# Performance work log

Measured on AMD Instinct MI355X. Metric: run time of the kernel, lower is better.

The kernel has to match this reference:

```python
import jax, jax.numpy as jnp
import numpy as np

SOM = (32, 32)   # som_dim; SOM[0]*SOM[1] == num_embeddings
LR = 0.05


def setup_inputs() -> dict:
    key = jax.random.key(0)
    k1, k2 = jax.random.split(key)
    B, K, D = 65536, 1024, 256
    x = jax.random.normal(k1, (B, D), dtype=jnp.float32)
    embeddings = jax.random.uniform(k2, (K, D), dtype=jnp.float32)  # torch.rand init
    return {"x": x, "embeddings": embeddings}


def reference(x, embeddings):
    K, D = embeddings.shape
    # pairwise squared distances: [B, K]
    dist = (jnp.sum(x * x, axis=1, keepdims=True)
            + jnp.sum(embeddings * embeddings, axis=1)
            - 2.0 * (x @ embeddings.T))
    n_min = jnp.argmin(dist, axis=1)          # [B]
    z_q = embeddings[n_min]                   # [B, D]

    # SOM grid coordinates and clamped neighbors
    n_x = n_min // SOM[1]
    n_y = n_min % SOM[1]
    x_up = jnp.where(n_x < SOM[0] - 1, n_x + 1, n_x)
    x_down = jnp.where(n_x > 0, n_x - 1, n_x)
    y_right = jnp.where(n_y < SOM[1] - 1, n_y + 1, n_y)
    y_left = jnp.where(n_y > 0, n_y - 1, n_y)
    idx_up = x_up * SOM[1] + n_y
    idx_down = x_down * SOM[1] + n_y
    idx_right = n_x * SOM[1] + y_right
    idx_left = n_x * SOM[1] + y_left

    # [B, 4, D] neighbor gather (order: up, down, left, right as in torch code)
    nbr_idx = jnp.stack([idx_up, idx_down, idx_left, idx_right], axis=1)
    z_q_neighbors = embeddings[nbr_idx]

    # SOM scatter update (torch does one-hot matmuls; segment_sum is the fused form)
    dw = x - z_q                              # [B, D]
    seg = lambda idx: jax.ops.segment_sum(dw, idx, num_segments=K)
    new_embeddings = jax.lax.stop_gradient(
        embeddings
        + LR * seg(n_min)
        + 0.5 * LR * (seg(idx_up) + seg(idx_down) + seg(idx_right) + seg(idx_left))
    )

    commit_loss = jnp.mean((x - z_q) ** 2)
    som_loss = jnp.mean((jax.lax.stop_gradient(x)[:, None, :] - z_q_neighbors) ** 2)
    return z_q, commit_loss, som_loss, new_embeddings
```

## Files before the change

kernel.cpp:

```cpp
#include <hip/hip_runtime.h>

#define B_ROWS 65536
#define DDIM   256
#define KEMB   1024
#define LRC    0.05f
#define BM 128

typedef __attribute__((ext_vector_type(8))) _Float16 half8;
typedef __attribute__((ext_vector_type(4))) float f32x4;

#define SX_OFF    0u
#define CNT_OFF   1048576u
#define SUMS_OFF  1052672u
#define ESQ_OFF   1053312u
#define CUR_OFF   1057408u
#define NMIN_OFF  1061504u
#define ROWS_OFF  1585792u
#define EH_OFF    1847936u

static __device__ __forceinline__ unsigned short f2h(float f) {
  _Float16 h = (_Float16)f;
  return *(unsigned short*)&h;
}
static __device__ __forceinline__ float h2f(unsigned short u) {
  _Float16 h = *(_Float16*)&u;
  return (float)h;
}
static __device__ __forceinline__ void glds16(const void* g, void* l) {
  __builtin_amdgcn_global_load_lds(
      (const __attribute__((address_space(1))) unsigned int*)g,
      (__attribute__((address_space(3))) unsigned int*)l, 16, 0, 0);
}

__global__ __launch_bounds__(256) void convert_kernel(
    const float* __restrict__ X, const float* __restrict__ E,
    unsigned short* __restrict__ outU, unsigned short* __restrict__ Eh,
    float* __restrict__ esq, double* __restrict__ sums) {
  __shared__ float red[256];
  const size_t nX8 = (size_t)B_ROWS * DDIM / 8;
  size_t i = (size_t)blockIdx.x * 256 + threadIdx.x;
  bool isX = (i < nX8);
  const float* src;
  unsigned short *dh, *dl = nullptr;
  if (isX) {
    size_t off = i * 8;
    src = X + off;
    dh = outU + (off >> 8) * 512 + (off & 255);
    dl = dh + 256;
  } else {
    size_t off = (i - nX8) * 8;
    src = E + off;
    dh = Eh + off;
  }
  const float4 v0 = *(const float4*)src;
  const float4 v1 = *(const float4*)(src + 4);
  float f[8] = {v0.x, v0.y, v0.z, v0.w, v1.x, v1.y, v1.z, v1.w};
  unsigned short h[8], l[8];
  float part = 0.f;
#pragma unroll
  for (int j = 0; j < 8; ++j) {
    h[j] = f2h(f[j]);
    l[j] = f2h(f[j] - h2f(h[j]));
    part += f[j] * f[j];
  }
  *(uint4*)dh = *(const uint4*)h;
  if (isX) *(uint4*)dl = *(const uint4*)l;
  if (!isX) {
    float s = part;
    for (int off = 16; off > 0; off >>= 1) s += __shfl_down(s, off, 32);
    if ((threadIdx.x & 31) == 0) esq[(i - nX8) >> 5] = s;
  }
  red[threadIdx.x] = isX ? part : 0.f;
  __syncthreads();
  for (int s = 128; s > 0; s >>= 1) {
    if (threadIdx.x < s) red[threadIdx.x] += red[threadIdx.x + s];
    __syncthreads();
  }
  if (threadIdx.x == 0 && isX)
    atomicAdd(&sums[8 + ((int)blockIdx.x & 63)], (double)red[0]);
}

__global__ __launch_bounds__(256, 1) void gemm_argmin_kernel(
    const unsigned short* __restrict__ XhlU, const unsigned short* __restrict__ EhW,
    const float* __restrict__ esq, const float* __restrict__ Ef,
    int* __restrict__ nmin, int* __restrict__ counts, float* __restrict__ zq) {
  __shared__ __align__(16) unsigned short sX[2][8][512][8];
  __shared__ __align__(16) unsigned short sE[2][512][8];

  const int tid  = threadIdx.x;
  const int lane = tid & 63, w = tid >> 6;
  const int lrow = lane & 15;
  const int qidx = lane >> 4;
  const int rowbase = (w >> 1) * 64;
  const int colb    = (w & 1) * 64;
  const int bm0 = (int)blockIdx.x * BM;

  int ec_row[2], ec_q8[2];
#pragma unroll
  for (int j = 0; j < 2; ++j) {
    const int c = j * 256 + tid;
    ec_row[j] = c >> 2;
    ec_q8[j]  = ((c & 3) ^ ((ec_row[j] >> 1) & 3)) * 8;
  }

#pragma unroll
  for (int j = 0; j < 2; ++j) {
    const int c = j * 256 + tid;
    glds16(EhW + (size_t)ec_row[j] * DDIM + ec_q8[j], (char*)&sE[0][c][0]);
  }
#pragma unroll
  for (int it = 0; it < 32; ++it) {
    const int c    = it * 256 + tid;
    const int tile = c >> 12;
    const int kcc  = (c >> 9) & 7;
    const int cc   = c & 511;
    const int row  = cc >> 2;
    const int q    = (cc & 3) ^ ((row >> 1) & 3);
    glds16(XhlU + (size_t)(bm0 + row) * 512 + tile * 256 + kcc * 32 + q * 8,
           (char*)sX + (size_t)c * 16);
  }

  float rbest[16];
  int   ridx[16];
#pragma unroll
  for (int i = 0; i < 16; ++i) { rbest[i] = 3.4e38f; ridx[i] = 0; }

  __syncthreads();

  for (int nt = 0; nt < 8; ++nt) {
    f32x4 acc[4][4];
#pragma unroll
    for (int i = 0; i < 4; ++i)
#pragma unroll
      for (int j = 0; j < 4; ++j) acc[i][j] = (f32x4){0.f, 0.f, 0.f, 0.f};

#pragma unroll
    for (int kcc = 0; kcc < 8; ++kcc) {
      const int s   = nt * 8 + kcc;
      const int cur = s & 1;
      if (s < 63) {
        const int ns = s + 1;
        const int nnt = ns >> 3, nk = ns & 7;
#pragma unroll
        for (int j = 0; j < 2; ++j) {
          const int c = j * 256 + tid;
          glds16(EhW + (size_t)(nnt * BM + ec_row[j]) * DDIM + nk * 32 + ec_q8[j],
                 (char*)&sE[cur ^ 1][c][0]);
        }
      }
      half8 af0[4], af1[4], bfr[4];
#pragma unroll
      for (int t = 0; t < 4; ++t) {
        const int m  = rowbase + t * 16 + lrow;
        const int sa = qidx ^ ((m >> 1) & 3);
        af0[t] = *(const half8*)&sX[0][kcc][(m << 2) | sa][0];
        af1[t] = *(const half8*)&sX[1][kcc][(m << 2) | sa][0];
        const int n  = colb + t * 16 + lrow;
        const int sb = qidx ^ ((n >> 1) & 3);
        bfr[t] = *(const half8*)&sE[cur][(n << 2) | sb][0];
      }
#pragma unroll
      for (int tr = 0; tr < 4; ++tr)
#pragma unroll
        for (int tc = 0; tc < 4; ++tc)
          acc[tr][tc] = __builtin_amdgcn_mfma_f32_16x16x32_f16(
              af0[tr], bfr[tc], acc[tr][tc], 0, 0, 0);
#pragma unroll
      for (int tr = 0; tr < 4; ++tr)
#pragma unroll
        for (int tc = 0; tc < 4; ++tc)
          acc[tr][tc] = __builtin_amdgcn_mfma_f32_16x16x32_f16(
              af1[tr], bfr[tc], acc[tr][tc], 0, 0, 0);
      __syncthreads();
    }
#pragma unroll
    for (int tc = 0; tc < 4; ++tc) {
      const int col = nt * BM + colb + tc * 16 + lrow;
      const float eq = esq[col];
#pragma unroll
      for (int tr = 0; tr < 4; ++tr)
#pragma unroll
        for (int rr = 0; rr < 4; ++rr) {
          float d = eq - 2.0f * acc[tr][tc][rr];
          const int slot = tr * 4 + rr;
          if (d < rbest[slot]) { rbest[slot] = d; ridx[slot] = col; }
        }
    }
  }

  float* cdd = (float*)&sE[0][0][0];
  int*   cdi = (int*)(cdd + 256);
  int*   snm = cdi + 256;
  int*   h   = (int*)&sX[0][0][0][0];

#pragma unroll
  for (int i = 0; i < 4; ++i) h[tid + i * 256] = 0;

#pragma unroll
  for (int slot = 0; slot < 16; ++slot) {
    float bd = rbest[slot];
    int   bi = ridx[slot];
#pragma unroll
    for (int off = 1; off < 16; off <<= 1) {
      float od = __shfl_xor(bd, off, 64);
      int   oi = __shfl_xor(bi, off, 64);
      if (od < bd || (od == bd && oi < bi)) { bd = od; bi = oi; }
    }
    if (lrow == 0) {
      const int row = rowbase + (slot >> 2) * 16 + (lane >> 4) * 4 + (slot & 3);
      cdd[(w & 1) * 128 + row] = bd;
      cdi[(w & 1) * 128 + row] = bi;
    }
  }
  __syncthreads();
  if (tid < BM) {
    float d0 = cdd[tid], d1 = cdd[128 + tid];
    int   i0 = cdi[tid], i1 = cdi[128 + tid];
    int bi = (d1 < d0 || (d1 == d0 && i1 < i0)) ? i1 : i0;
    nmin[bm0 + tid] = bi;
    snm[tid] = bi;
    atomicAdd(&h[bi], 1);
  }
  __syncthreads();
#pragma unroll
  for (int i = 0; i < 4; ++i) {
    int v = h[tid + i * 256];
    if (v) atomicAdd(&counts[tid + i * 256], v);
  }
  const int r0 = w * 32;
#pragma unroll 4
  for (int r = 0; r < 32; ++r) {
    const int k = snm[r0 + r];
    const float4 v = *(const float4*)(Ef + (size_t)k * DDIM + lane * 4);
    *(float4*)(zq + (size_t)(bm0 + r0 + r) * DDIM + lane * 4) = v;
  }
}

__global__ __launch_bounds__(1024) void scan_kernel(
    const int* __restrict__ counts, int* __restrict__ cur) {
  __shared__ int tmp[KEMB];
  int tid = threadIdx.x;
  int v = counts[tid];
  tmp[tid] = v;
  __syncthreads();
  for (int off = 1; off < 1024; off <<= 1) {
    int u = (tid >= off) ? tmp[tid - off] : 0;
    __syncthreads();
    tmp[tid] += u;
    __syncthreads();
  }
  cur[tid] = tmp[tid] - v;
}

__global__ __launch_bounds__(1024) void scatter_kernel(
    const int* __restrict__ nm, int* __restrict__ cur,
    int* __restrict__ rows) {
  __shared__ int lcnt[KEMB], lbase[KEMB], lrank[KEMB];
  int tid = threadIdx.x;
  lcnt[tid] = 0; lrank[tid] = 0;
  __syncthreads();
  int b = blockIdx.x * 1024 + tid;
  int k = nm[b];
  atomicAdd(&lcnt[k], 1);
  __syncthreads();
  if (lcnt[tid] > 0) lbase[tid] = atomicAdd(&cur[tid], lcnt[tid]);
  __syncthreads();
  int r = atomicAdd(&lrank[k], 1);
  rows[lbase[k] + r] = b;
}

__global__ __launch_bounds__(256) void sxsum_kernel(
    const int* __restrict__ rows, const int* __restrict__ nm,
    const float* __restrict__ X, float* __restrict__ SX) {
  __shared__ int sb[64], sk[64];
  int tid = threadIdx.x;
  int p0 = blockIdx.x * 64;
  if (tid < 64) sb[tid] = rows[p0 + tid];
  __syncthreads();
  if (tid < 64) sk[tid] = nm[sb[tid]];
  __syncthreads();
  float acc = 0.f;
  int kprev = sk[0];
  for (int i = 0; i < 64; ++i) {
    int k = sk[i];
    if (k != kprev) {
      atomicAdd(&SX[(size_t)kprev * DDIM + tid], acc);
      acc = 0.f;
      kprev = k;
    }
    acc += X[(size_t)sb[i] * DDIM + tid];
  }
  atomicAdd(&SX[(size_t)kprev * DDIM + tid], acc);
}

__global__ __launch_bounds__(256) void stencil_kernel(
    const float* __restrict__ E, const float* __restrict__ SX,
    const int* __restrict__ counts, const float* __restrict__ esq,
    double* __restrict__ sums, float* __restrict__ out) {
  __shared__ float redc[256], reds[256];
  int k = blockIdx.x, t = threadIdx.x;
  int kx = k >> 5, ky = k & 31;
  int j1 = (kx >= 1)  ? k - 32 : k;
  int j2 = (kx <= 30) ? k + 32 : k;
  int j3 = (ky >= 1)  ? k - 1  : k;
  int j4 = (ky <= 30) ? k + 1  : k;
  int fU = (kx < 31) ? k + 32 : k;
  int fD = (kx > 0)  ? k - 32 : k;
  int fL = (ky > 0)  ? k - 1  : k;
  int fR = (ky < 31) ? k + 1  : k;

  float e   = E[(size_t)k * DDIM + t];
  float sxk = SX[(size_t)k * DDIM + t];
  float Tk = sxk - (float)counts[k] * e;
  float T1 = SX[(size_t)j1 * DDIM + t] - (float)counts[j1] * E[(size_t)j1 * DDIM + t];
  float T2 = SX[(size_t)j2 * DDIM + t] - (float)counts[j2] * E[(size_t)j2 * DDIM + t];
  float T3 = SX[(size_t)j3 * DDIM + t] - (float)counts[j3] * E[(size_t)j3 * DDIM + t];
  float T4 = SX[(size_t)j4 * DDIM + t] - (float)counts[j4] * E[(size_t)j4 * DDIM + t];
  float v = e + LRC * Tk + 0.5f * LRC * (T1 + T2 + T3 + T4);
  out[(size_t)B_ROWS * DDIM + 2 + (size_t)k * DDIM + t] = v;

  float eU = E[(size_t)fU * DDIM + t], eD = E[(size_t)fD * DDIM + t];
  float eL = E[(size_t)fL * DDIM + t], eR = E[(size_t)fR * DDIM + t];
  float cp = -2.f * sxk * e;
  float sp = -2.f * sxk * (eU + eD + eL + eR);
  if (t == 0) {
    float ck = (float)counts[k];
    cp += ck * esq[k];
    sp += ck * (esq[fU] + esq[fD] + esq[fL] + esq[fR]);
  }
  redc[t] = cp; reds[t] = sp;
  __syncthreads();
  for (int s = 128; s > 0; s >>= 1) {
    if (t < s) { redc[t] += redc[t + s]; reds[t] += reds[t + s]; }
    __syncthreads();
  }
  if (t == 0) {
    atomicAdd(&sums[1], (double)redc[0]);
    atomicAdd(&sums[2], (double)reds[0]);
  }
}

__global__ void finalize_kernel(const double* __restrict__ sums,
                                float* __restrict__ out) {
  double xsq = 0.0;
  for (int s = 0; s < 64; ++s) xsq += sums[8 + s];
  out[(size_t)B_ROWS * DDIM]     = (float)((xsq + sums[1]) / ((double)B_ROWS * DDIM));
  out[(size_t)B_ROWS * DDIM + 1] =
      (float)((4.0 * xsq + sums[2]) / ((double)B_ROWS * 4.0 * DDIM));
}

extern "C" void kernel_launch(void* const* d_in, const int* in_sizes, int n_in,
                              void* d_out, int out_size, void* d_ws, size_t ws_size,
                              hipStream_t stream) {
  const float* X = (const float*)d_in[0];
  const float* E = (const float*)d_in[1];
  float* out = (float*)d_out;
  unsigned short* outU = (unsigned short*)d_out;
  char* ws = (char*)d_ws;

  float*          SX   = (float*)(ws + SX_OFF);
  int*            cnts = (int*)(ws + CNT_OFF);
  double*         sums = (double*)(ws + SUMS_OFF);
  float*          esq  = (float*)(ws + ESQ_OFF);
  int*            cur  = (int*)(ws + CUR_OFF);
  int*            nm   = (int*)(ws + NMIN_OFF);
  int*            rows = (int*)(ws + ROWS_OFF);
  unsigned short* EhW  = (unsigned short*)(ws + EH_OFF);

  hipMemsetAsync(ws, 0, ESQ_OFF, stream);

  convert_kernel<<<(B_ROWS * (DDIM / 8) + KEMB * (DDIM / 8)) / 256, 256, 0, stream>>>(
      X, E, outU, EhW, esq, sums);
  gemm_argmin_kernel<<<B_ROWS / BM, 256, 0, stream>>>(outU, EhW, esq, E, nm, cnts, out);
  scan_kernel<<<1, 1024, 0, stream>>>(cnts, cur);
  scatter_kernel<<<B_ROWS / 1024, 1024, 0, stream>>>(nm, cur, rows);
  sxsum_kernel<<<B_ROWS / 64, 256, 0, stream>>>(rows, nm, X, SX);
  stencil_kernel<<<KEMB, 256, 0, stream>>>(E, SX, cnts, esq, sums, out);
  finalize_kernel<<<1, 1, 0, stream>>>(sums, out);
}
```

Measured before the change: 309.7 us.

## Triple-buffer embedding tiles and prefetch LDS fragments one step ahead

Grows the shared-memory embedding staging buffer from two to three slots, so global-to-LDS loads run two k-steps ahead. MFMA operand fragments for the next step are read from LDS into registers (ping-pong fA/gA sets) while the current step's MFMAs run. The full __syncthreads per step becomes an explicit vmcnt(0) wait plus s_barrier. This is meant to hide LDS and global latency behind matrix math, at the cost of more registers and LDS, which may limit occupancy or cause spills.

```diff
diff --git a/kernel.cpp b/kernel.cpp
--- a/kernel.cpp
+++ b/kernel.cpp
@@ -85,7 +85,7 @@
     const float* __restrict__ esq, const float* __restrict__ Ef,
     int* __restrict__ nmin, int* __restrict__ counts, float* __restrict__ zq) {
   __shared__ __align__(16) unsigned short sX[2][8][512][8];
-  __shared__ __align__(16) unsigned short sE[2][512][8];
+  __shared__ __align__(16) unsigned short sE[3][512][8];
 
   const int tid  = threadIdx.x;
   const int lane = tid & 63, w = tid >> 6;
@@ -104,10 +104,11 @@
   }
 
 #pragma unroll
-  for (int j = 0; j < 2; ++j) {
-    const int c = j * 256 + tid;
-    glds16(EhW + (size_t)ec_row[j] * DDIM + ec_q8[j], (char*)&sE[0][c][0]);
-  }
+  for (int j = 0; j < 2; ++j)
+    glds16(EhW + (size_t)ec_row[j] * DDIM + ec_q8[j], (char*)&sE[0][j * 256 + tid][0]);
+#pragma unroll
+  for (int j = 0; j < 2; ++j)
+    glds16(EhW + (size_t)ec_row[j] * DDIM + 32 + ec_q8[j], (char*)&sE[1][j * 256 + tid][0]);
 #pragma unroll
   for (int it = 0; it < 32; ++it) {
     const int c    = it * 256 + tid;
@@ -125,69 +126,89 @@
 #pragma unroll
   for (int i = 0; i < 16; ++i) { rbest[i] = 3.4e38f; ridx[i] = 0; }
 
-  __syncthreads();
-
-  for (int nt = 0; nt < 8; ++nt) {
-    f32x4 acc[4][4];
-#pragma unroll
-    for (int i = 0; i < 4; ++i)
-#pragma unroll
-      for (int j = 0; j < 4; ++j) acc[i][j] = (f32x4){0.f, 0.f, 0.f, 0.f};
-
-#pragma unroll
-    for (int kcc = 0; kcc < 8; ++kcc) {
-      const int s   = nt * 8 + kcc;
-      const int cur = s & 1;
-      if (s < 63) {
-        const int ns = s + 1;
-        const int nnt = ns >> 3, nk = ns & 7;
-#pragma unroll
-        for (int j = 0; j < 2; ++j) {
-          const int c = j * 256 + tid;
-          glds16(EhW + (size_t)(nnt * BM + ec_row[j]) * DDIM + nk * 32 + ec_q8[j],
-                 (char*)&sE[cur ^ 1][c][0]);
-        }
-      }
-      half8 af0[4], af1[4], bfr[4];
-#pragma unroll
-      for (int t = 0; t < 4; ++t) {
-        const int m  = rowbase + t * 16 + lrow;
-        const int sa = qidx ^ ((m >> 1) & 3);
-        af0[t] = *(const half8*)&sX[0][kcc][(m << 2) | sa][0];
-        af1[t] = *(const half8*)&sX[1][kcc][(m << 2) | sa][0];
-        const int n  = colb + t * 16 + lrow;
-        const int sb = qidx ^ ((n >> 1) & 3);
-        bfr[t] = *(const half8*)&sE[cur][(n << 2) | sb][0];
-      }
-#pragma unroll
-      for (int tr = 0; tr < 4; ++tr)
-#pragma unroll
-        for (int tc = 0; tc < 4; ++tc)
-          acc[tr][tc] = __builtin_amdgcn_mfma_f32_16x16x32_f16(
-              af0[tr], bfr[tc], acc[tr][tc], 0, 0, 0);
-#pragma unroll
-      for (int tr = 0; tr < 4; ++tr)
-#pragma unroll
-        for (int tc = 0; tc < 4; ++tc)
-          acc[tr][tc] = __builtin_amdgcn_mfma_f32_16x16x32_f16(
-              af1[tr], bfr[tc], acc[tr][tc], 0, 0, 0);
-      __syncthreads();
-    }
-#pragma unroll
-    for (int tc = 0; tc < 4; ++tc) {
-      const int col = nt * BM + colb + tc * 16 + lrow;
-      const float eq = esq[col];
-#pragma unroll
-      for (int tr = 0; tr < 4; ++tr)
-#pragma unroll
-        for (int rr = 0; rr < 4; ++rr) {
-          float d = eq - 2.0f * acc[tr][tc][rr];
-          const int slot = tr * 4 + rr;
-          if (d < rbest[slot]) { rbest[slot] = d; ridx[slot] = col; }
-        }
-    }
-  }
-
+  int ra[4], rb[4];
+#pragma unroll
+  for (int t = 0; t < 4; ++t) {
+    const int m = rowbase + t * 16 + lrow;
+    ra[t] = (m << 2) | (qidx ^ ((m >> 1) & 3));
+    const int n = colb + t * 16 + lrow;
+    rb[t] = (n << 2) | (qidx ^ ((n >> 1) & 3));
+  }
+
+  __syncthreads();
+
+  half8 fA0[4], fA1[4], fB[4], gA0[4], gA1[4], gB[4];
+#pragma unroll
+  for (int t = 0; t < 4; ++t) {
+    fA0[t] = *(const half8*)&sX[0][0][ra[t]][0];
+    fA1[t] = *(const half8*)&sX[1][0][ra[t]][0];
+    fB[t]  = *(const half8*)&sE[0][rb[t]][0];
+  }
+
+  f32x4 acc[4][4];
+  int rbuf = 1;
+  int wbuf = 2;
+
+#define PIPE_STEP(c0, c1, cB, n0, n1, nB, S)                                     \
+  {                                                                              \
+    const int s_ = (S);                                                          \
+    if ((s_ & 7) == 0) {                                                         \
+      _Pragma("unroll") for (int i_ = 0; i_ < 4; ++i_)                           \
+        _Pragma("unroll") for (int j_ = 0; j_ < 4; ++j_)                         \
+          acc[i_][j_] = (f32x4){0.f, 0.f, 0.f, 0.f};                             \
+    }                                                                            \
+    if (s_ + 2 < 64) {   \
+      const int se_ = s_ + 2, nnt_ = se_ >> 3, nk_ = se_ & 7;                    \
+      _Pragma("unroll") for (int j_ = 0; j_ < 2; ++j_) {                         \
+        const int c_ = j_ * 256 + tid;                                           \
+        glds16(EhW + (size_t)(nnt_ * BM + ec_row[j_]) * DDIM + nk_ * 32 +        \
+                   ec_q8[j_],                                                    \
+               (char*)&sE[wbuf][c_][0]);                                         \
+      }                                                                          \
+    }                                                                            \
+    if (s_ + 1 < 64) {       \
+      const int k1_ = (s_ + 1) & 7;                                              \
+      _Pragma("unroll") for (int t_ = 0; t_ < 4; ++t_) {                         \
+        n0[t_] = *(const half8*)&sX[0][k1_][ra[t_]][0];                          \
+        n1[t_] = *(const half8*)&sX[1][k1_][ra[t_]][0];                          \
+        nB[t_] = *(const half8*)&sE[rbuf][rb[t_]][0];                            \
+      }                                                                          \
+    }                                                                            \
+    _Pragma("unroll") for (int tr_ = 0; tr_ < 4; ++tr_)                          \
+      _Pragma("unroll") for (int tc_ = 0; tc_ < 4; ++tc_)                        \
+        acc[tr_][tc_] = __builtin_amdgcn_mfma_f32_16x16x32_f16(                  \
+            c0[tr_], cB[tc_], acc[tr_][tc_], 0, 0, 0);                           \
+    _Pragma("unroll") for (int tr_ = 0; tr_ < 4; ++tr_)                          \
+      _Pragma("unroll") for (int tc_ = 0; tc_ < 4; ++tc_)                        \
+        acc[tr_][tc_] = __builtin_amdgcn_mfma_f32_16x16x32_f16(                  \
+            c1[tr_], cB[tc_], acc[tr_][tc_], 0, 0, 0);                           \
+    if ((s_ & 7) == 7) {    \
+      const int nt_ = s_ >> 3;                                                   \
+      _Pragma("unroll") for (int tc_ = 0; tc_ < 4; ++tc_) {                      \
+        const int col_ = nt_ * BM + colb + tc_ * 16 + lrow;                      \
+        const float eq_ = esq[col_];                                             \
+        _Pragma("unroll") for (int tr_ = 0; tr_ < 4; ++tr_)                      \
+          _Pragma("unroll") for (int rr_ = 0; rr_ < 4; ++rr_) {                  \
+            float d_ = eq_ - 2.0f * acc[tr_][tc_][rr_];                          \
+            const int sl_ = tr_ * 4 + rr_;                                       \
+            if (d_ < rbest[sl_]) { rbest[sl_] = d_; ridx[sl_] = col_; }          \
+          }                                                                      \
+      }                                                                          \
+    }                                                                            \
+    rbuf = (rbuf == 2) ? 0 : rbuf + 1;                                           \
+    wbuf = (wbuf == 2) ? 0 : wbuf + 1;                                           \
+    asm volatile("s_waitcnt vmcnt(0)" ::: "memory");   \
+    __builtin_amdgcn_s_barrier();                                                \
+  }
+
+  for (int sp = 0; sp < 32; ++sp) {
+    const int s0 = sp * 2;
+    PIPE_STEP(fA0, fA1, fB, gA0, gA1, gB, s0);
+    PIPE_STEP(gA0, gA1, gB, fA0, fA1, fB, s0 + 1);
+  }
+#undef PIPE_STEP
+
+  __syncthreads();
   float* cdd = (float*)&sE[0][0][0];
   int*   cdi = (int*)(cdd + 256);
   int*   snm = cdi + 256;
```

Measured after the change: 327.3 us. 1.06x slower.
